# Kernel optimization log

Hardware: AMD Instinct MI355X
Metric: run time of the kernel (lower is better)

## Reference

```python
import jax, jax.numpy as jnp
import numpy as np

MAX_PATCH = 8   # max_patch_size: fixed span length
D_MODEL = 128
VOCAB = 256     # byte vocabulary
B, T = 16, 16384


def setup_inputs() -> dict:
    key = jax.random.key(0)
    k1, k2 = jax.random.split(key)
    x_u8 = jax.random.randint(k1, (B, T), 0, VOCAB, dtype=jnp.int32)
    byte_embed = jax.random.normal(k2, (VOCAB, D_MODEL), dtype=jnp.float32)
    return {"x_u8": x_u8, "byte_embed": byte_embed}


def reference(x_u8, byte_embed):
    # heuristic='fixed': spans are contiguous chunks of MAX_PATCH bytes.
    # Per span: embedding lookup then mean over the span -> [B, Tp, D].
    b, t = x_u8.shape
    tp = t // MAX_PATCH  # T divisible by MAX_PATCH (no ragged tail)
    emb = byte_embed[x_u8]  # gather: [B, T, D]
    out = emb.reshape(b, tp, MAX_PATCH, D_MODEL).mean(axis=2)  # [B, Tp, D]
    return out
```

## Files before the change

kernel.cpp:

```cpp
#include <hip/hip_runtime.h>
#include <hip/hip_bf16.h>


#define NPATCH  32768
#define TPB     1024
#define NBLK    256
#define GROUPS_PER_BLOCK (TPB / 32)
#define NGROUPS (NBLK * GROUPS_PER_BLOCK)
#define ITERS   (NPATCH / NGROUPS)

__global__ __launch_bounds__(TPB, 1) void blt_patch_mean_lds(
    const int4* __restrict__ x4,
    const float4* __restrict__ emb4,
    float4* __restrict__ out4)
{
    __shared__ float4 tbl[8192];

    {
        const float4* gsrc = emb4 + threadIdx.x;
        float4*       ldst = tbl  + threadIdx.x;
        #pragma unroll
        for (int i = 0; i < 8; ++i) {
            __builtin_amdgcn_global_load_lds(
                (const __attribute__((address_space(1))) unsigned int*)(gsrc + i * TPB),
                (__attribute__((address_space(3))) unsigned int*)(ldst + i * TPB),
                16, 0, 0);
        }
    }

    const int group0 = (int)blockIdx.x * GROUPS_PER_BLOCK + ((int)threadIdx.x >> 5);
    const int col    = threadIdx.x & 31;
    const float s    = 0.125f;

    {
        const int p = group0;
        int4 i0 = x4[p * 2];
        int4 i1 = x4[p * 2 + 1];
        float4 acc = make_float4(0.f, 0.f, 0.f, 0.f);
        #define ACCUMG(r) { float4 v = emb4[(r) * 32 + col];                   \
                            acc.x += v.x; acc.y += v.y; acc.z += v.z; acc.w += v.w; }
        ACCUMG(i0.x); ACCUMG(i0.y); ACCUMG(i0.z); ACCUMG(i0.w);
        ACCUMG(i1.x); ACCUMG(i1.y); ACCUMG(i1.z); ACCUMG(i1.w);
        #undef ACCUMG
        acc.x *= s; acc.y *= s; acc.z *= s; acc.w *= s;
        out4[p * 32 + col] = acc;
    }

    __syncthreads();

    #pragma unroll
    for (int it = 1; it < ITERS; ++it) {
        const int p = group0 + it * NGROUPS;
        int4 i0 = x4[p * 2];
        int4 i1 = x4[p * 2 + 1];
        float4 acc = make_float4(0.f, 0.f, 0.f, 0.f);
        #define ACCUM(r) { float4 v = tbl[(r) * 32 + col];                     \
                           acc.x += v.x; acc.y += v.y; acc.z += v.z; acc.w += v.w; }
        ACCUM(i0.x); ACCUM(i0.y); ACCUM(i0.z); ACCUM(i0.w);
        ACCUM(i1.x); ACCUM(i1.y); ACCUM(i1.z); ACCUM(i1.w);
        #undef ACCUM
        acc.x *= s; acc.y *= s; acc.z *= s; acc.w *= s;
        out4[p * 32 + col] = acc;
    }
}

extern "C" void kernel_launch(void* const* d_in, const int* in_sizes, int n_in,
                              void* d_out, int out_size, void* d_ws, size_t ws_size,
                              hipStream_t stream)
{
    const int4*   x4   = (const int4*)d_in[0];
    const float4* emb4 = (const float4*)d_in[1];
    float4*       out4 = (float4*)d_out;

    blt_patch_mean_lds<<<NBLK, TPB, 0, stream>>>(x4, emb4, out4);
}
```

Measured before the change: 12.55 us.

## Prefetch all patch indices before LDS sync and use nontemporal output stores

All index loads for the block's four iterations are issued up front, so they overlap with the async copy of the embedding table into LDS. The first iteration, which previously gathered straight from global memory before the barrier, now waits and reads from LDS like the others. Output stores become nontemporal to limit cache pollution from the streaming write. In exchange, the first iteration can no longer overlap with the table load, and more index registers stay live.

```diff
diff --git a/kernel.cpp b/kernel.cpp
--- a/kernel.cpp
+++ b/kernel.cpp
@@ -5,11 +5,13 @@
 #define NPATCH  32768
 #define TPB     1024
 #define NBLK    256
-#define GROUPS_PER_BLOCK (TPB / 32)
-#define NGROUPS (NBLK * GROUPS_PER_BLOCK)
+#define GPB     (TPB / 32)
+#define NGROUPS (NBLK * GPB)
 #define ITERS   (NPATCH / NGROUPS)
 
-__global__ __launch_bounds__(TPB, 1) void blt_patch_mean_lds(
+typedef float nfloat4 __attribute__((ext_vector_type(4)));
+
+__global__ __launch_bounds__(TPB, 1) void blt_patch_mean_r4(
     const int4* __restrict__ x4,
     const float4* __restrict__ emb4,
     float4* __restrict__ out4)
@@ -28,39 +30,32 @@
         }
     }
 
-    const int group0 = (int)blockIdx.x * GROUPS_PER_BLOCK + ((int)threadIdx.x >> 5);
+    const int group0 = (int)blockIdx.x * GPB + ((int)threadIdx.x >> 5);
     const int col    = threadIdx.x & 31;
     const float s    = 0.125f;
 
-    {
-        const int p = group0;
-        int4 i0 = x4[p * 2];
-        int4 i1 = x4[p * 2 + 1];
-        float4 acc = make_float4(0.f, 0.f, 0.f, 0.f);
-        #define ACCUMG(r) { float4 v = emb4[(r) * 32 + col];                   \
-                            acc.x += v.x; acc.y += v.y; acc.z += v.z; acc.w += v.w; }
-        ACCUMG(i0.x); ACCUMG(i0.y); ACCUMG(i0.z); ACCUMG(i0.w);
-        ACCUMG(i1.x); ACCUMG(i1.y); ACCUMG(i1.z); ACCUMG(i1.w);
-        #undef ACCUMG
-        acc.x *= s; acc.y *= s; acc.z *= s; acc.w *= s;
-        out4[p * 32 + col] = acc;
+    int4 ia[ITERS], ib[ITERS];
+    #pragma unroll
+    for (int it = 0; it < ITERS; ++it) {
+        const int p = group0 + it * NGROUPS;
+        ia[it] = x4[p * 2];
+        ib[it] = x4[p * 2 + 1];
     }
 
     __syncthreads();
 
     #pragma unroll
-    for (int it = 1; it < ITERS; ++it) {
+    for (int it = 0; it < ITERS; ++it) {
         const int p = group0 + it * NGROUPS;
-        int4 i0 = x4[p * 2];
-        int4 i1 = x4[p * 2 + 1];
         float4 acc = make_float4(0.f, 0.f, 0.f, 0.f);
         #define ACCUM(r) { float4 v = tbl[(r) * 32 + col];                     \
                            acc.x += v.x; acc.y += v.y; acc.z += v.z; acc.w += v.w; }
-        ACCUM(i0.x); ACCUM(i0.y); ACCUM(i0.z); ACCUM(i0.w);
-        ACCUM(i1.x); ACCUM(i1.y); ACCUM(i1.z); ACCUM(i1.w);
+        ACCUM(ia[it].x); ACCUM(ia[it].y); ACCUM(ia[it].z); ACCUM(ia[it].w);
+        ACCUM(ib[it].x); ACCUM(ib[it].y); ACCUM(ib[it].z); ACCUM(ib[it].w);
         #undef ACCUM
         acc.x *= s; acc.y *= s; acc.z *= s; acc.w *= s;
-        out4[p * 32 + col] = acc;
+        nfloat4 v = { acc.x, acc.y, acc.z, acc.w };
+        __builtin_nontemporal_store(v, (nfloat4*)&out4[p * 32 + col]);
     }
 }
 
@@ -72,5 +67,5 @@
     const float4* emb4 = (const float4*)d_in[1];
     float4*       out4 = (float4*)d_out;
 
-    blt_patch_mean_lds<<<NBLK, TPB, 0, stream>>>(x4, emb4, out4);
+    blt_patch_mean_r4<<<NBLK, TPB, 0, stream>>>(x4, emb4, out4);
 }
```

Measured after the change: 11.80 us. 6.0% less time.
